# Kernel tuning notes

Hardware: AMD Instinct MI355X
Metric: run time of the kernel (lower is better)

The kernel has to match this reference:

```python
import jax, jax.numpy as jnp
import numpy as np

HOP = 768
NCB = 14
DIM = 512
VOCAB = 1024
W_SCALE = 0.02  # keep conv stacks numerically tame


def conv1d(x, w, b, stride=1, padding=0):
    # x: [B,C,L], w: [O,I,K] (torch layout), b: [O]
    y = jax.lax.conv_general_dilated(
        x, w, window_strides=(stride,), padding=[(padding, padding)],
        dimension_numbers=('NCH', 'OIH', 'NCH'))
    return y + b[None, :, None]


def conv_transpose1d(x, w, b, stride, padding):
    # torch ConvTranspose1d weight layout: (in, out, k)
    k = w.shape[2]
    w2 = jnp.flip(jnp.transpose(w, (1, 0, 2)), axis=2)  # -> OIH
    y = jax.lax.conv_general_dilated(
        x, w2, window_strides=(1,),
        padding=[(k - 1 - padding, k - 1 - padding)],
        lhs_dilation=(stride,),
        dimension_numbers=('NCH', 'OIH', 'NCH'))
    return y + b[None, :, None]


def setup_inputs() -> dict:
    key = jax.random.key(0)
    ks = jax.random.split(key, 16)
    f = lambda k, shp, s=W_SCALE: jax.random.normal(k, shp, dtype=jnp.float32) * s
    B, T = 2, 98304  # T = 768 * 128
    return {
        'audio': jax.random.normal(ks[0], (B, 1, T), dtype=jnp.float32),
        'codebooks': jax.random.normal(ks[1], (NCB, VOCAB, DIM), dtype=jnp.float32),
        'ew1': f(ks[2], (256, 1, 7)), 'eb1': f(ks[3], (256,)),
        'ew2': f(ks[4], (512, 256, 5)), 'eb2': f(ks[5], (512,)),
        'ew3': f(ks[6], (NCB * DIM, 512, 3)), 'eb3': f(ks[7], (NCB * DIM,)),
        'dw1': f(ks[8], (NCB * DIM, 512, 5)), 'db1': f(ks[9], (512,)),
        'dw2': f(ks[10], (256, 512, 5)), 'db2': f(ks[11], (256,)),
        'dw3': f(ks[12], (1, 256, 7)), 'db3': f(ks[13], (1,)),
    }


def reference(audio, codebooks, ew1, eb1, ew2, eb2, ew3, eb3,
              dw1, db1, dw2, db2, dw3, db3):
    B = audio.shape[0]
    # ---- encoder ----
    h = jax.nn.relu(conv1d(audio, ew1, eb1, stride=1, padding=3))
    h = jax.nn.relu(conv1d(h, ew2, eb2, stride=HOP, padding=2))
    h = conv1d(h, ew3, eb3, stride=1, padding=1)          # [B, NCB*DIM, S]
    S = h.shape[-1]
    emb = h.reshape(B, NCB, DIM, S).transpose(0, 1, 3, 2)  # [B, NCB, S, DIM]
    # ---- VQ: per-codebook squared L2 distance + argmin (same argmin as cdist) ----
    d2 = (jnp.sum(emb * emb, axis=-1, keepdims=True)            # [B,NCB,S,1]
          - 2.0 * jnp.einsum('bksd,kvd->bksv', emb, codebooks)  # [B,NCB,S,V]
          + jnp.sum(codebooks * codebooks, axis=-1)[None, :, None, :])
    codes = jnp.argmin(d2, axis=-1)                        # [B, NCB, S] int
    # ---- decode: embedding lookup + transposed conv decoder ----
    q = codebooks[jnp.arange(NCB)[None, :, None], codes]   # [B, NCB, S, DIM]
    q = q.transpose(0, 1, 3, 2).reshape(B, NCB * DIM, S)   # [B, NCB*DIM, S]
    a = jax.nn.relu(conv_transpose1d(q, dw1, db1, stride=HOP, padding=2))
    a = jax.nn.relu(conv1d(a, dw2, db2, stride=1, padding=2))
    a = jnp.tanh(conv1d(a, dw3, db3, stride=1, padding=3))
    return a  # [B, 1, (S-1)*HOP + 1]
```

## Files before the change

kernel.cpp:

```cpp
#include <hip/hip_runtime.h>
#include <hip/hip_bf16.h>
#include <math.h>

#define T_IN 98304
#define SS 128
#define NBATCH 2
#define NN 256
#define C1 256
#define C2 512
#define C3 7168
#define NCBK 14
#define DIMV 512
#define VOC 1024
#define TOUT 97537
#define HOP 768

#define OFF_CBN    0L
#define OFF_AB1    14336L
#define OFF_AB2    14848L
#define OFF_CCONST 15104L
#define OFF_H2C    15120L
#define OFF_H2XH   146192L
#define OFF_H2XL   342800L
#define OFF_H3H    539408L
#define OFF_H3L    1456912L
#define OFF_X1H    2374416L
#define OFF_X1L    2538256L
#define OFF_DW1T   539408L
#define OFF_XH     539408L
#define OFF_XL     3488528L
#define OFF_CODES  9714448L
#define OFF_QBF    9718032L
#define OFF_A1RAW  10635536L
#define OFF_DW2PH  10635536L
#define OFF_DW2PL  10963216L
#define OFF_A2ACT  11290896L
#define OFF_CBPH   11880720L
#define OFF_CBPL   15550736L
#define OFF_EW3PH  19220752L
#define OFF_EW3PL  24725776L
#define OFF_EW2PH  30230800L
#define OFF_EW2PL  30558480L
#define OFF_PVAL   30886160L
#define OFF_PIDX   30943504L

typedef __attribute__((ext_vector_type(8))) short short8;
typedef __attribute__((ext_vector_type(4))) float f32x4;

static __device__ inline ushort f2bf(float x) {
  __hip_bfloat16 h = __float2bfloat16(x);
  return *reinterpret_cast<ushort*>(&h);
}

static __device__ inline void split8(const float4 x0, const float4 x1,
                                     short8& h, short8& l) {
  float xs[8] = {x0.x, x0.y, x0.z, x0.w, x1.x, x1.y, x1.z, x1.w};
  #pragma unroll
  for (int e = 0; e < 8; ++e) {
    uint b = __float_as_uint(xs[e]);
    h[e] = (short)(b >> 16);
    float r = xs[e] - __uint_as_float(b & 0xffff0000u);
    l[e] = (short)(__float_as_uint(r) >> 16);
  }
}

__global__ __launch_bounds__(256) void k_cbp(const float* __restrict__ cb,
    ushort* __restrict__ ph, ushort* __restrict__ pl, float* __restrict__ cbn) {
  __shared__ float red[256];
  int zmt = blockIdx.x;
  int t = threadIdx.x;
  int lane = t & 63, fg = t >> 6;
  int quad = lane >> 4, l15 = lane & 15;
  int row = zmt * 16 + l15;
  float ss = 0.f;
  #pragma unroll
  for (int h = 0; h < 4; ++h) {
    int kt = fg * 4 + h;
    int k = kt * 32 + quad * 8;
    const float* s = cb + (long)row * DIMV + k;
    float4 x0 = *(const float4*)s;
    float4 x1 = *(const float4*)(s + 4);
    short8 hh, ll;
    split8(x0, x1, hh, ll);
    long off = ((long)zmt * 16 + kt) * 512 + lane * 8;
    *(short8*)(ph + off) = hh;
    *(short8*)(pl + off) = ll;
    ss += x0.x*x0.x + x0.y*x0.y + x0.z*x0.z + x0.w*x0.w
        + x1.x*x1.x + x1.y*x1.y + x1.z*x1.z + x1.w*x1.w;
  }
  red[t] = ss;
  __syncthreads();
  if (t < 16) {
    float s = 0.f;
    #pragma unroll
    for (int g = 0; g < 16; ++g) s += red[t + g * 16];
    cbn[zmt * 16 + t] = s;
  }
}

__global__ __launch_bounds__(256) void k_prep_ab2(const float* __restrict__ db1,
    const float* __restrict__ dw2, const float* __restrict__ db2,
    float* __restrict__ ab1, float* __restrict__ ab2) {
  __shared__ float red[256];
  int o = blockIdx.x, t = threadIdx.x;
  if (o == 0) { ab1[t] = fmaxf(db1[t], 0.f); ab1[t + 256] = fmaxf(db1[t + 256], 0.f); }
  const float* wp = dw2 + (long)o * C2 * 5;
  float acc = 0.f;
  #pragma unroll
  for (int h = 0; h < 2; ++h) {
    int c = t + h * 256;
    const float* p = wp + c * 5;
    float wsum = p[0] + p[1] + p[2] + p[3] + p[4];
    acc = fmaf(wsum, fmaxf(db1[c], 0.f), acc);
  }
  red[t] = acc;
  __syncthreads();
  for (int off = 128; off; off >>= 1) {
    if (t < off) red[t] += red[t + off];
    __syncthreads();
  }
  if (t == 0) ab2[o] = fmaxf(red[0] + db2[o], 0.f);
}

__global__ __launch_bounds__(256) void k_prep_c(const float* __restrict__ dw3,
    const float* __restrict__ db3, const float* __restrict__ ab2,
    float* __restrict__ cconst) {
  __shared__ float red[256];
  int t = threadIdx.x;
  float wsum3 = 0.f;
  #pragma unroll
  for (int j = 0; j < 7; ++j) wsum3 += dw3[t*7+j];
  red[t] = wsum3 * ab2[t];
  __syncthreads();
  for (int off = 128; off; off >>= 1) {
    if (t < off) red[t] += red[t + off];
    __syncthreads();
  }
  if (t == 0) cconst[0] = tanhf(red[0] + db3[0]);
}

__global__ __launch_bounds__(256) void k_enc1(const float* __restrict__ audio,
    const float* __restrict__ ew1, const float* __restrict__ eb1,
    ushort* __restrict__ X1h, ushort* __restrict__ X1l) {
  int n = blockIdx.x, ic = threadIdx.x;
  int b = n >> 7, s = n & 127;
  const float* ap = audio + (long)b * T_IN;
  int base = HOP * s - 5;
  float a[11];
  #pragma unroll
  for (int w = 0; w < 11; ++w) {
    int ai = base + w;
    a[w] = (ai >= 0 && ai < T_IN) ? ap[ai] : 0.f;
  }
  float w1[7];
  #pragma unroll
  for (int j = 0; j < 7; ++j) w1[j] = ew1[ic*7+j];
  float b1 = eb1[ic];
  #pragma unroll
  for (int jj = 0; jj < 5; ++jj) {
    int tcol = HOP * s + jj - 2;
    float v = 0.f;
    if (tcol >= 0) {
      float acc = b1;
      #pragma unroll
      for (int j = 0; j < 7; ++j) acc = fmaf(w1[j], a[jj + j], acc);
      v = fmaxf(acc, 0.f);
    }
    int k = ic * 5 + jj;
    int kt = k >> 5;
    int lane2 = ((k >> 3) & 3) * 16 + (n & 15);
    long idx = ((long)((n >> 4) * 40 + kt)) * 512 + lane2 * 8 + (k & 7);
    uint bi = __float_as_uint(v);
    X1h[idx] = (ushort)(bi >> 16);
    float r = v - __uint_as_float(bi & 0xffff0000u);
    X1l[idx] = (ushort)(__float_as_uint(r) >> 16);
  }
}

__global__ __launch_bounds__(256) void k_ew2p(const float* __restrict__ ew2,
    ushort* __restrict__ ph, ushort* __restrict__ pl) {
  int o8 = blockIdx.x * 256 + threadIdx.x;
  const int total = 512 * 1280 / 8;
  if (o8 >= total) return;
  int frag = o8 >> 6, lane = o8 & 63;
  int quad = lane >> 4, l15 = lane & 15;
  int mt = frag / 40, kt = frag - mt * 40;
  int m = mt * 16 + l15;
  int k = kt * 32 + quad * 8;
  const float* s = ew2 + (long)m * 1280 + k;
  float4 x0 = *(const float4*)s;
  float4 x1 = *(const float4*)(s + 4);
  short8 h, l;
  split8(x0, x1, h, l);
  long off = (long)o8 * 8;
  *(short8*)(ph + off) = h;
  *(short8*)(pl + off) = l;
}

__global__ __launch_bounds__(256) void gemm_enc2(const ushort* __restrict__ aH,
    const ushort* __restrict__ aL, const ushort* __restrict__ bH,
    const ushort* __restrict__ bL, const float* __restrict__ eb2,
    float* __restrict__ h2c) {
  __shared__ __align__(16) float red[4 * 2048];
  const int tid = threadIdx.x;
  const int w = tid >> 6, lane = tid & 63;
  const int l15 = lane & 15, quad = lane >> 4;
  const int m0 = blockIdx.x * 32, n0 = blockIdx.y * 64;
  const int mt0 = blockIdx.x * 2, nt0 = blockIdx.y * 4;
  const int kt0 = w * 10;
  f32x4 acc[2][4] = {};
  const ushort* aHB = aH + ((long)(mt0 * 40 + kt0)) * 512 + lane * 8;
  const ushort* aLB = aL + ((long)(mt0 * 40 + kt0)) * 512 + lane * 8;
  const ushort* bHB = bH + ((long)(nt0 * 40 + kt0)) * 512 + lane * 8;
  const ushort* bLB = bL + ((long)(nt0 * 40 + kt0)) * 512 + lane * 8;
  for (int kt = 0; kt < 10; ++kt) {
    short8 ah[2], al[2], bh[4], bl[4];
    #pragma unroll
    for (int i = 0; i < 2; ++i) {
      long o = ((long)(i * 40 + kt)) * 512;
      ah[i] = *(const short8*)(aHB + o);
      al[i] = *(const short8*)(aLB + o);
    }
    #pragma unroll
    for (int f = 0; f < 4; ++f) {
      long o = ((long)(f * 40 + kt)) * 512;
      bh[f] = *(const short8*)(bHB + o);
      bl[f] = *(const short8*)(bLB + o);
    }
    #pragma unroll
    for (int i = 0; i < 2; ++i)
      #pragma unroll
      for (int j = 0; j < 4; ++j) {
        acc[i][j] = __builtin_amdgcn_mfma_f32_16x16x32_bf16(ah[i], bh[j], acc[i][j], 0, 0, 0);
        acc[i][j] = __builtin_amdgcn_mfma_f32_16x16x32_bf16(ah[i], bl[j], acc[i][j], 0, 0, 0);
        acc[i][j] = __builtin_amdgcn_mfma_f32_16x16x32_bf16(al[i], bh[j], acc[i][j], 0, 0, 0);
      }
  }
  #pragma unroll
  for (int i = 0; i < 2; ++i)
    #pragma unroll
    for (int j = 0; j < 4; ++j)
      *(float4*)&red[w * 2048 + (i * 4 + j) * 256 + lane * 4] = *(float4*)&acc[i][j];
  __syncthreads();
  #pragma unroll
  for (int q = 0; q < 2; ++q) {
    const int c = 2 * w + q;
    const int i = c >> 2, j = c & 3;
    float4 s = make_float4(0.f, 0.f, 0.f, 0.f);
    #pragma unroll
    for (int g = 0; g < 4; ++g) {
      float4 t4 = *(const float4*)&red[g * 2048 + c * 256 + lane * 4];
      s.x += t4.x; s.y += t4.y; s.z += t4.z; s.w += t4.w;
    }
    const int obase = m0 + i * 16 + quad * 4;
    float4 bias = *(const float4*)(eb2 + obase);
    const int n = n0 + j * 16 + l15;
    float4 out;
    out.x = fmaxf(s.x + bias.x, 0.f);
    out.y = fmaxf(s.y + bias.y, 0.f);
    out.z = fmaxf(s.z + bias.z, 0.f);
    out.w = fmaxf(s.w + bias.w, 0.f);
    *(float4*)(h2c + (long)n * C2 + obase) = out;
  }
}

__global__ void k_h2x(const float* __restrict__ h2c, ushort* __restrict__ h2xph,
                      ushort* __restrict__ h2xpl) {
  int idx = blockIdx.x * 256 + threadIdx.x;
  const int total = NN * 1536;
  for (; idx < total; idx += gridDim.x * 256) {
    int grp = idx >> 9;
    int r = idx & 511;
    int e = r & 7, lane = r >> 3;
    int quad = lane >> 4, l15 = lane & 15;
    int nt = grp / 48, kt = grp - nt * 48;
    int n = nt * 16 + l15;
    int k = kt * 32 + quad * 8 + e;
    int ic = k / 3, j = k - ic * 3;
    int s2 = (n & 127) + j - 1;
    int b = n >> 7;
    float v = (s2 >= 0 && s2 < SS) ? h2c[(long)(b*SS + s2)*C2 + ic] : 0.f;
    uint bi = __float_as_uint(v);
    h2xph[idx] = (ushort)(bi >> 16);
    float rr = v - __uint_as_float(bi & 0xffff0000u);
    h2xpl[idx] = (ushort)(__float_as_uint(rr) >> 16);
  }
}

__global__ __launch_bounds__(256) void k_ew3p(const float* __restrict__ ew3,
    ushort* __restrict__ ph, ushort* __restrict__ pl) {
  int o8 = blockIdx.x * 256 + threadIdx.x;
  const int total = C3 * 1536 / 8;
  if (o8 >= total) return;
  int frag = o8 >> 6, lane = o8 & 63;
  int quad = lane >> 4, l15 = lane & 15;
  int mtL = frag / 48, kt = frag - mtL * 48;
  int m = mtL * 16 + l15;
  int k = kt * 32 + quad * 8;
  const float* s = ew3 + (long)m * 1536 + k;
  float4 x0 = *(const float4*)s;
  float4 x1 = *(const float4*)(s + 4);
  short8 h, l;
  split8(x0, x1, h, l);
  long off = (long)o8 * 8;
  *(short8*)(ph + off) = h;
  *(short8*)(pl + off) = l;
}

__global__ __launch_bounds__(256) void gemm_h3(const ushort* __restrict__ aH,
    const ushort* __restrict__ aL, const ushort* __restrict__ bH,
    const ushort* __restrict__ bL, const float* __restrict__ eb3,
    ushort* __restrict__ h3ph, ushort* __restrict__ h3pl) {
  __shared__ __align__(16) float red[4 * 4096];
  const int tid = threadIdx.x;
  const int w = tid >> 6, lane = tid & 63;
  const int l15 = lane & 15, quad = lane >> 4;
  const int bid = blockIdx.x;
  const int xcd = bid & 7, q = bid >> 3;
  const int mchunk = xcd * 14 + (q >> 2);
  const int nchunk = q & 3;
  const int mtL0 = mchunk * 4, nt0 = nchunk * 4, n0 = nchunk * 64;
  const int kt0 = w * 12;
  f32x4 acc[4][4] = {};
  const ushort* aHB = aH + ((long)(mtL0 * 48 + kt0)) * 512 + lane * 8;
  const ushort* aLB = aL + ((long)(mtL0 * 48 + kt0)) * 512 + lane * 8;
  const ushort* bHB = bH + ((long)(nt0 * 48 + kt0)) * 512 + lane * 8;
  const ushort* bLB = bL + ((long)(nt0 * 48 + kt0)) * 512 + lane * 8;
  for (int kt = 0; kt < 12; ++kt) {
    short8 ah[4], al[4], bh[4], bl[4];
    #pragma unroll
    for (int f = 0; f < 4; ++f) {
      long o = ((long)(f * 48 + kt)) * 512;
      ah[f] = *(const short8*)(aHB + o);
      al[f] = *(const short8*)(aLB + o);
      bh[f] = *(const short8*)(bHB + o);
      bl[f] = *(const short8*)(bLB + o);
    }
    #pragma unroll
    for (int i = 0; i < 4; ++i)
      #pragma unroll
      for (int j = 0; j < 4; ++j) {
        acc[i][j] = __builtin_amdgcn_mfma_f32_16x16x32_bf16(ah[i], bh[j], acc[i][j], 0, 0, 0);
        acc[i][j] = __builtin_amdgcn_mfma_f32_16x16x32_bf16(ah[i], bl[j], acc[i][j], 0, 0, 0);
        acc[i][j] = __builtin_amdgcn_mfma_f32_16x16x32_bf16(al[i], bh[j], acc[i][j], 0, 0, 0);
      }
  }
  #pragma unroll
  for (int i = 0; i < 4; ++i)
    #pragma unroll
    for (int j = 0; j < 4; ++j)
      *(float4*)&red[w * 4096 + (i * 4 + j) * 256 + lane * 4] = *(float4*)&acc[i][j];
  __syncthreads();
  const int mg0 = mchunk * 64 + w * 16 + quad * 4;
  float4 bias = *(const float4*)(eb3 + mg0);
  const int ktS = mg0 >> 5, quadk = (mg0 >> 3) & 3, es = mg0 & 7;
  #pragma unroll
  for (int j = 0; j < 4; ++j) {
    float4 s = *(const float4*)&red[(w * 4 + j) * 256 + lane * 4];
    #pragma unroll
    for (int r = 1; r < 4; ++r) {
      float4 tt = *(const float4*)&red[r * 4096 + (w * 4 + j) * 256 + lane * 4];
      s.x += tt.x; s.y += tt.y; s.z += tt.z; s.w += tt.w;
    }
    const int n = n0 + j * 16 + l15;
    float v0 = s.x + bias.x;
    float v1 = s.y + bias.y;
    float v2 = s.z + bias.z;
    float v3 = s.w + bias.w;
    uint b0 = __float_as_uint(v0), b1 = __float_as_uint(v1);
    uint b2 = __float_as_uint(v2), b3 = __float_as_uint(v3);
    uint2 hp;
    hp.x = (b0 >> 16) | (b1 & 0xffff0000u);
    hp.y = (b2 >> 16) | (b3 & 0xffff0000u);
    float r0 = v0 - __uint_as_float(b0 & 0xffff0000u);
    float r1 = v1 - __uint_as_float(b1 & 0xffff0000u);
    float r2 = v2 - __uint_as_float(b2 & 0xffff0000u);
    float r3 = v3 - __uint_as_float(b3 & 0xffff0000u);
    uint2 lp;
    lp.x = (__float_as_uint(r0) >> 16) | (__float_as_uint(r1) & 0xffff0000u);
    lp.y = (__float_as_uint(r2) >> 16) | (__float_as_uint(r3) & 0xffff0000u);
    long off = ((long)((n >> 4) * 224 + ktS)) * 512 + (quadk * 16 + (n & 15)) * 8 + es;
    *(uint2*)(h3ph + off) = hp;
    *(uint2*)(h3pl + off) = lp;
  }
}

__global__ __launch_bounds__(256) void gemm_scores(const ushort* __restrict__ aH,
    const ushort* __restrict__ aL, const ushort* __restrict__ bH,
    const ushort* __restrict__ bL, const float* __restrict__ cbn,
    float* __restrict__ pval, int* __restrict__ pidx) {
  __shared__ __align__(16) float red[4 * 4096];
  __shared__ float wv_[4 * 64];
  __shared__ int   wi_[4 * 64];
  const int tid = threadIdx.x;
  const int w = tid >> 6, lane = tid & 63;
  const int l15 = lane & 15, quad = lane >> 4;
  const int m0 = blockIdx.x * 64, n0 = blockIdx.y * 64, z = blockIdx.z;
  const int mt0 = blockIdx.x * 4;
  const int kt0 = w * 4;
  f32x4 acc[4][4] = {};
  const ushort* aHB = aH + ((long)((z * 64 + mt0) * 16 + kt0)) * 512 + lane * 8;
  const ushort* aLB = aL + ((long)((z * 64 + mt0) * 16 + kt0)) * 512 + lane * 8;
  const ushort* bHB = bH + ((long)((n0 >> 4) * 224 + z * 16 + kt0)) * 512 + lane * 8;
  const ushort* bLB = bL + ((long)((n0 >> 4) * 224 + z * 16 + kt0)) * 512 + lane * 8;
  for (int kt = 0; kt < 4; ++kt) {
    short8 ah[4], al[4], bh[4], bl[4];
    #pragma unroll
    for (int f = 0; f < 4; ++f) {
      long oa = ((long)(f * 16 + kt)) * 512;
      long ob = ((long)(f * 224 + kt)) * 512;
      ah[f] = *(const short8*)(aHB + oa);
      al[f] = *(const short8*)(aLB + oa);
      bh[f] = *(const short8*)(bHB + ob);
      bl[f] = *(const short8*)(bLB + ob);
    }
    #pragma unroll
    for (int i = 0; i < 4; ++i)
      #pragma unroll
      for (int j = 0; j < 4; ++j) {
        acc[i][j] = __builtin_amdgcn_mfma_f32_16x16x32_bf16(ah[i], bh[j], acc[i][j], 0, 0, 0);
        acc[i][j] = __builtin_amdgcn_mfma_f32_16x16x32_bf16(ah[i], bl[j], acc[i][j], 0, 0, 0);
        acc[i][j] = __builtin_amdgcn_mfma_f32_16x16x32_bf16(al[i], bh[j], acc[i][j], 0, 0, 0);
      }
  }
  #pragma unroll
  for (int i = 0; i < 4; ++i)
    #pragma unroll
    for (int j = 0; j < 4; ++j)
      *(float4*)&red[w * 4096 + (i * 4 + j) * 256 + lane * 4] = *(float4*)&acc[i][j];
  __syncthreads();
  const int vbase = m0 + w * 16 + quad * 4;
  float4 cn = *(const float4*)(cbn + z * VOC + vbase);
  #pragma unroll
  for (int j = 0; j < 4; ++j) {
    float4 s = *(const float4*)&red[(w * 4 + j) * 256 + lane * 4];
    #pragma unroll
    for (int r = 1; r < 4; ++r) {
      float4 tt = *(const float4*)&red[r * 4096 + (w * 4 + j) * 256 + lane * 4];
      s.x += tt.x; s.y += tt.y; s.z += tt.z; s.w += tt.w;
    }
    float o0 = cn.x - 2.f * s.x;
    float o1 = cn.y - 2.f * s.y;
    float o2 = cn.z - 2.f * s.z;
    float o3 = cn.w - 2.f * s.w;
    float bv = o0; int bm = vbase;
    if (o1 < bv) { bv = o1; bm = vbase + 1; }
    if (o2 < bv) { bv = o2; bm = vbase + 2; }
    if (o3 < bv) { bv = o3; bm = vbase + 3; }
    #pragma unroll
    for (int off = 16; off <= 32; off <<= 1) {
      float ov = __shfl_xor(bv, off);
      int om = __shfl_xor(bm, off);
      if (ov < bv || (ov == bv && om < bm)) { bv = ov; bm = om; }
    }
    if (quad == 0) { wv_[w * 64 + j * 16 + l15] = bv; wi_[w * 64 + j * 16 + l15] = bm; }
  }
  __syncthreads();
  if (tid < 64) {
    float bv = wv_[tid]; int bm = wi_[tid];
    #pragma unroll
    for (int g = 1; g < 4; ++g) {
      float ov = wv_[g * 64 + tid]; int om = wi_[g * 64 + tid];
      if (ov < bv || (ov == bv && om < bm)) { bv = ov; bm = om; }
    }
    long prow = (long)z * NN + n0 + tid;
    pval[prow * 16 + blockIdx.x] = bv;
    pidx[prow * 16 + blockIdx.x] = bm;
  }
}

__global__ void k_argmin2(const float* __restrict__ pval, const int* __restrict__ pidx,
                          int* __restrict__ codes) {
  int row = blockIdx.x * 256 + threadIdx.x;
  if (row >= NCBK * NN) return;
  const float* pv = pval + (long)row * 16;
  const int*   pi = pidx + (long)row * 16;
  float bv = pv[0]; int bm = pi[0];
  #pragma unroll
  for (int c = 1; c < 16; ++c) {
    float v = pv[c]; int m = pi[c];
    if (v < bv || (v == bv && m < bm)) { bv = v; bm = m; }
  }
  codes[row] = bm;
}

__global__ __launch_bounds__(256) void k_dw1t(const float* __restrict__ dw1,
                                              ushort* __restrict__ dw1p) {
  __shared__ __align__(16) ushort T[64 * 72];
  int t = threadIdx.x;
  int k0 = blockIdx.x * 64, m0 = blockIdx.y * 64;
  int kk = t >> 2, mj = (t & 3) * 16;
  const float* src = dw1 + (long)(k0 + kk) * 2560 + m0 + mj;
  float x[16];
  *(float4*)&x[0]  = *(const float4*)(src);
  *(float4*)&x[4]  = *(const float4*)(src + 4);
  *(float4*)&x[8]  = *(const float4*)(src + 8);
  *(float4*)&x[12] = *(const float4*)(src + 12);
  #pragma unroll
  for (int l = 0; l < 16; ++l)
    T[(mj + l) * 72 + kk] = f2bf(x[l]);
  __syncthreads();
  int mo = t >> 2, kc = (t & 3) * 16;
  const int m = m0 + mo;
  const int mt = m >> 4, l15 = m & 15;
  #pragma unroll
  for (int h = 0; h < 2; ++h) {
    const int kk0 = kc + h * 8;
    const int kglob = k0 + kk0;
    const int kt = kglob >> 5;
    const int quad = (kglob >> 3) & 3;
    uint4 u = *(const uint4*)&T[mo * 72 + kk0];
    *(uint4*)(dw1p + ((long)(mt * 224 + kt)) * 512 + (quad * 16 + l15) * 8) = u;
  }
}

__global__ void k_gather_qbf(const float* __restrict__ cb, const int* __restrict__ codes,
                             ushort* __restrict__ qp) {
  int o = blockIdx.x * 256 + threadIdx.x;
  const int total = NN * C3 / 8;
  if (o >= total) return;
  int frag = o >> 6, r = o & 63;
  int quad = r >> 4, l15 = r & 15;
  int nt = frag / 224, kt = frag - nt * 224;
  int n = nt * 16 + l15;
  int kglob = kt * 32 + quad * 8;
  int kcb = kglob >> 9, d0 = kglob & 511;
  int code = codes[kcb * NN + n];
  const float* s = cb + ((long)(kcb * VOC + code)) * DIMV + d0;
  float4 x0 = *(const float4*)s;
  float4 x1 = *(const float4*)(s + 4);
  uint4 u;
  u.x = (uint)f2bf(x0.x) | ((uint)f2bf(x0.y) << 16);
  u.y = (uint)f2bf(x0.z) | ((uint)f2bf(x0.w) << 16);
  u.z = (uint)f2bf(x1.x) | ((uint)f2bf(x1.y) << 16);
  u.w = (uint)f2bf(x1.z) | ((uint)f2bf(x1.w) << 16);
  ((uint4*)qp)[o] = u;
}

__global__ __launch_bounds__(1024) void gemm_a1_mfma(const ushort* __restrict__ dw1p,
    const ushort* __restrict__ qp, float* __restrict__ a1raw) {
  __shared__ __align__(16) float red[4 * 4096];
  const int tid = threadIdx.x;
  const int w = tid >> 6, lane = tid & 63;
  const int l15 = lane & 15, quad = lane >> 4;
  const int mt0 = blockIdx.x * 4, nt0 = blockIdx.y * 4;
  const int kt0 = w * 14;
  f32x4 acc[4][4] = {};
  const ushort* aB = dw1p + ((long)(mt0 * 224 + kt0)) * 512 + lane * 8;
  const ushort* bB = qp   + ((long)(nt0 * 224 + kt0)) * 512 + lane * 8;
  #pragma unroll 2
  for (int kt = 0; kt < 14; ++kt) {
    short8 ah[4], bh[4];
    #pragma unroll
    for (int f = 0; f < 4; ++f) {
      ah[f] = *(const short8*)(aB + ((long)(f * 224 + kt)) * 512);
      bh[f] = *(const short8*)(bB + ((long)(f * 224 + kt)) * 512);
    }
    #pragma unroll
    for (int i = 0; i < 4; ++i)
      #pragma unroll
      for (int j = 0; j < 4; ++j)
        acc[i][j] = __builtin_amdgcn_mfma_f32_16x16x32_bf16(ah[i], bh[j], acc[i][j], 0, 0, 0);
  }
  float4 rsum = make_float4(0.f, 0.f, 0.f, 0.f);
  #pragma unroll
  for (int r = 0; r < 4; ++r) {
    if ((w >> 2) == r) {
      #pragma unroll
      for (int i = 0; i < 4; ++i)
        #pragma unroll
        for (int j = 0; j < 4; ++j)
          *(float4*)&red[(w & 3) * 4096 + (i * 4 + j) * 256 + lane * 4] = *(float4*)&acc[i][j];
    }
    __syncthreads();
    #pragma unroll
    for (int g = 0; g < 4; ++g) {
      float4 t4 = *(const float4*)&red[g * 4096 + w * 256 + lane * 4];
      rsum.x += t4.x; rsum.y += t4.y; rsum.z += t4.z; rsum.w += t4.w;
    }
    __syncthreads();
  }
  const int ci = w >> 2, cj = w & 3;
  const int n = nt0 * 16 + cj * 16 + l15;
  const int mb = mt0 * 16 + ci * 16 + quad * 4;
  float v[4] = {rsum.x, rsum.y, rsum.z, rsum.w};
  #pragma unroll
  for (int reg = 0; reg < 4; ++reg) {
    int m = mb + reg;
    int c = m / 5, jj = m - c * 5;
    a1raw[((long)(n * 5 + jj)) * C2 + c] = v[reg];
  }
}

__global__ void k_x2(const float* __restrict__ a1raw, const float* __restrict__ ab1g,
                     const float* __restrict__ db1, ushort* __restrict__ Xh,
                     ushort* __restrict__ Xl) {
  int idx = blockIdx.x * 256 + threadIdx.x;
  const int total = 2304 * 2560;
  for (; idx < total; idx += gridDim.x * 256) {
    int grp = idx >> 9;
    int r = idx & 511;
    int e = r & 7, lane = r >> 3;
    int quad = lane >> 4, l15 = lane & 15;
    int nt = grp / 80, kt = grp - nt * 80;
    int nu = nt * 16 + l15;
    int ck = kt * 32 + quad * 8 + e;
    int n = nu / 9, u = nu - n * 9;
    int c = ck / 5, jj = ck - c * 5;
    int w = u + jj;
    int s = n & 127;
    int tc = HOP * s - 6 + w;
    float v;
    if (tc < 0 || tc > TOUT - 1) v = 0.f;
    else if (w >= 4 && w <= 8)
      v = fmaxf(db1[c] + a1raw[((long)(n * 5 + (w - 4))) * C2 + c], 0.f);
    else v = ab1g[c];
    uint bi = __float_as_uint(v);
    Xh[idx] = (ushort)(bi >> 16);
    float rr = v - __uint_as_float(bi & 0xffff0000u);
    Xl[idx] = (ushort)(__float_as_uint(rr) >> 16);
  }
}

__global__ __launch_bounds__(256) void k_dw2p(const float* __restrict__ dw2,
    ushort* __restrict__ ph, ushort* __restrict__ pl) {
  int o8 = blockIdx.x * 256 + threadIdx.x;
  const int total = 256 * 2560 / 8;
  if (o8 >= total) return;
  int frag = o8 >> 6, lane = o8 & 63;
  int quad = lane >> 4, l15 = lane & 15;
  int mt = frag / 80, kt = frag - mt * 80;
  int m = mt * 16 + l15;
  int k = kt * 32 + quad * 8;
  const float* s = dw2 + (long)m * 2560 + k;
  float4 x0 = *(const float4*)s;
  float4 x1 = *(const float4*)(s + 4);
  short8 h, l;
  split8(x0, x1, h, l);
  long off = (long)o8 * 8;
  *(short8*)(ph + off) = h;
  *(short8*)(pl + off) = l;
}

__global__ __launch_bounds__(256) void gemm_dec2(const ushort* __restrict__ aH,
    const ushort* __restrict__ aL, const ushort* __restrict__ bH,
    const ushort* __restrict__ bL, const float* __restrict__ db2,
    float* __restrict__ a2act) {
  __shared__ __align__(16) float red[4 * 4096];
  const int tid = threadIdx.x;
  const int w = tid >> 6, lane = tid & 63;
  const int l15 = lane & 15, quad = lane >> 4;
  const int mt0 = blockIdx.x * 4, nt0 = blockIdx.y * 4;
  const int m0 = mt0 * 16, n0 = nt0 * 16;
  const int kt0 = w * 20;
  f32x4 acc[4][4] = {};
  const ushort* aHB = aH + ((long)(mt0 * 80 + kt0)) * 512 + lane * 8;
  const ushort* aLB = aL + ((long)(mt0 * 80 + kt0)) * 512 + lane * 8;
  const ushort* bHB = bH + ((long)(nt0 * 80 + kt0)) * 512 + lane * 8;
  const ushort* bLB = bL + ((long)(nt0 * 80 + kt0)) * 512 + lane * 8;
  for (int kt = 0; kt < 20; ++kt) {
    short8 ah[4], al[4], bh[4], bl[4];
    #pragma unroll
    for (int f = 0; f < 4; ++f) {
      long o = ((long)(f * 80 + kt)) * 512;
      ah[f] = *(const short8*)(aHB + o);
      al[f] = *(const short8*)(aLB + o);
      bh[f] = *(const short8*)(bHB + o);
      bl[f] = *(const short8*)(bLB + o);
    }
    #pragma unroll
    for (int i = 0; i < 4; ++i)
      #pragma unroll
      for (int j = 0; j < 4; ++j) {
        acc[i][j] = __builtin_amdgcn_mfma_f32_16x16x32_bf16(ah[i], bh[j], acc[i][j], 0, 0, 0);
        acc[i][j] = __builtin_amdgcn_mfma_f32_16x16x32_bf16(ah[i], bl[j], acc[i][j], 0, 0, 0);
        acc[i][j] = __builtin_amdgcn_mfma_f32_16x16x32_bf16(al[i], bh[j], acc[i][j], 0, 0, 0);
      }
  }
  #pragma unroll
  for (int i = 0; i < 4; ++i)
    #pragma unroll
    for (int j = 0; j < 4; ++j)
      *(float4*)&red[w * 4096 + (i * 4 + j) * 256 + lane * 4] = *(float4*)&acc[i][j];
  __syncthreads();
  const int mb = m0 + w * 16 + quad * 4;
  float4 bias = *(const float4*)(db2 + mb);
  #pragma unroll
  for (int j = 0; j < 4; ++j) {
    float4 s = *(const float4*)&red[(w * 4 + j) * 256 + lane * 4];
    #pragma unroll
    for (int r = 1; r < 4; ++r) {
      float4 tt = *(const float4*)&red[r * 4096 + (w * 4 + j) * 256 + lane * 4];
      s.x += tt.x; s.y += tt.y; s.z += tt.z; s.w += tt.w;
    }
    const int nu = n0 + j * 16 + l15;
    float4 out;
    out.x = fmaxf(s.x + bias.x, 0.f);
    out.y = fmaxf(s.y + bias.y, 0.f);
    out.z = fmaxf(s.z + bias.z, 0.f);
    out.w = fmaxf(s.w + bias.w, 0.f);
    *(float4*)(a2act + (long)nu * C1 + mb) = out;
  }
}

__global__ void k_fill(float* __restrict__ outp, const float* __restrict__ cconst) {
  float v = cconst[0];
  int idx = blockIdx.x * 256 + threadIdx.x;
  const int total = NBATCH * TOUT;
  for (; idx < total; idx += gridDim.x * 256) outp[idx] = v;
}

__global__ __launch_bounds__(256) void k_dec3(const float* __restrict__ a2act,
    const float* __restrict__ ab2g, const float* __restrict__ dw3,
    const float* __restrict__ db3, float* __restrict__ outp) {
  __shared__ float sa2[9 * C1];
  __shared__ float sb[C1];
  int n = blockIdx.x;
  int s = n & 127, b = n >> 7;
  int t = threadIdx.x;
  for (int i = t; i < 9 * C1; i += 256) sa2[i] = a2act[(long)n * 9 * C1 + i];
  sb[t] = ab2g[t];
  __syncthreads();
  int wv = t >> 6, lane = t & 63;
  float b3 = db3[0];
  for (int w15 = wv; w15 < 15; w15 += 4) {
    int tc = HOP * s - 7 + w15;
    if (tc < 0 || tc > TOUT - 1) continue;
    float part = 0.f;
    for (int cc = lane; cc < C1; cc += 64) {
      #pragma unroll
      for (int j = 0; j < 7; ++j) {
        int wcol = tc + j - 3;
        float x;
        if (wcol < 0 || wcol > TOUT - 1) x = 0.f;
        else {
          int du = wcol - (HOP * s - 4);
          x = (du >= 0 && du <= 8) ? sa2[du * C1 + cc] : sb[cc];
        }
        part = fmaf(dw3[cc*7+j], x, part);
      }
    }
    for (int off = 32; off; off >>= 1) part += __shfl_down(part, off);
    if (lane == 0) outp[(long)b * TOUT + tc] = tanhf(part + b3);
  }
}

extern "C" void kernel_launch(void* const* d_in, const int* in_sizes, int n_in,
                              void* d_out, int out_size, void* d_ws, size_t ws_size,
                              hipStream_t stream) {
  const float* audio = (const float*)d_in[0];
  const float* cb    = (const float*)d_in[1];
  const float* ew1   = (const float*)d_in[2];
  const float* eb1   = (const float*)d_in[3];
  const float* ew2   = (const float*)d_in[4];
  const float* eb2   = (const float*)d_in[5];
  const float* ew3   = (const float*)d_in[6];
  const float* eb3   = (const float*)d_in[7];
  const float* dw1   = (const float*)d_in[8];
  const float* db1   = (const float*)d_in[9];
  const float* dw2   = (const float*)d_in[10];
  const float* db2   = (const float*)d_in[11];
  const float* dw3   = (const float*)d_in[12];
  const float* db3   = (const float*)d_in[13];
  float* outp = (float*)d_out;
  float* ws = (float*)d_ws;

  float*  cbn    = ws + OFF_CBN;
  float*  ab1    = ws + OFF_AB1;
  float*  ab2    = ws + OFF_AB2;
  float*  cconst = ws + OFF_CCONST;
  float*  h2c    = ws + OFF_H2C;
  ushort* h2xph  = (ushort*)(ws + OFF_H2XH);
  ushort* h2xpl  = (ushort*)(ws + OFF_H2XL);
  ushort* h3ph   = (ushort*)(ws + OFF_H3H);
  ushort* h3pl   = (ushort*)(ws + OFF_H3L);
  ushort* X1h    = (ushort*)(ws + OFF_X1H);
  ushort* X1l    = (ushort*)(ws + OFF_X1L);
  ushort* cbph   = (ushort*)(ws + OFF_CBPH);
  ushort* cbpl   = (ushort*)(ws + OFF_CBPL);
  ushort* ew3ph  = (ushort*)(ws + OFF_EW3PH);
  ushort* ew3pl  = (ushort*)(ws + OFF_EW3PL);
  ushort* ew2ph  = (ushort*)(ws + OFF_EW2PH);
  ushort* ew2pl  = (ushort*)(ws + OFF_EW2PL);
  float*  pval   = ws + OFF_PVAL;
  int*    pidx   = (int*)(ws + OFF_PIDX);
  ushort* dw1p   = (ushort*)(ws + OFF_DW1T);
  ushort* Xh     = (ushort*)(ws + OFF_XH);
  ushort* Xl     = (ushort*)(ws + OFF_XL);
  int*    codes  = (int*)(ws + OFF_CODES);
  ushort* qp     = (ushort*)(ws + OFF_QBF);
  float*  a1raw  = ws + OFF_A1RAW;
  ushort* dw2ph  = (ushort*)(ws + OFF_DW2PH);
  ushort* dw2pl  = (ushort*)(ws + OFF_DW2PL);
  float*  a2act  = ws + OFF_A2ACT;

  k_cbp<<<896, 256, 0, stream>>>(cb, cbph, cbpl, cbn);
  k_prep_ab2<<<C1, 256, 0, stream>>>(db1, dw2, db2, ab1, ab2);
  k_prep_c<<<1, 256, 0, stream>>>(dw3, db3, ab2, cconst);
  k_enc1<<<NN, 256, 0, stream>>>(audio, ew1, eb1, X1h, X1l);
  k_ew2p<<<320, 256, 0, stream>>>(ew2, ew2ph, ew2pl);
  gemm_enc2<<<dim3(16, 4), 256, 0, stream>>>(ew2ph, ew2pl, X1h, X1l, eb2, h2c);
  k_h2x<<<384, 256, 0, stream>>>(h2c, h2xph, h2xpl);
  k_ew3p<<<5376, 256, 0, stream>>>(ew3, ew3ph, ew3pl);
  gemm_h3<<<448, 256, 0, stream>>>(ew3ph, ew3pl, h2xph, h2xpl, eb3, h3ph, h3pl);
  gemm_scores<<<dim3(16, 4, 14), 256, 0, stream>>>(cbph, cbpl, h3ph, h3pl, cbn, pval, pidx);
  k_argmin2<<<14, 256, 0, stream>>>(pval, pidx, codes);
  k_dw1t<<<dim3(112, 40), 256, 0, stream>>>(dw1, dw1p);
  k_gather_qbf<<<896, 256, 0, stream>>>(cb, codes, qp);
  gemm_a1_mfma<<<dim3(40, 4), 1024, 0, stream>>>(dw1p, qp, a1raw);
  k_x2<<<4096, 256, 0, stream>>>(a1raw, ab1, db1, Xh, Xl);
  k_dw2p<<<320, 256, 0, stream>>>(dw2, dw2ph, dw2pl);
  gemm_dec2<<<dim3(4, 36), 256, 0, stream>>>(dw2ph, dw2pl, Xh, Xl, db2, a2act);
  k_fill<<<256, 256, 0, stream>>>(outp, cconst);
  k_dec3<<<NN, 256, 0, stream>>>(a2act, ab2, dw3, db3, outp);
}
```

Baseline: 389.3 us.

## Merge weight-packing kernels, fuse output fill into dec3, widen dec2 split-K

The five separate weight-packing kernels (codebook, ew2, ew3, dw2, dw1 transpose) are merged into one large launch that branches on block index, and their workspace regions are moved so they no longer alias. The standalone constant-fill kernel is folded into k_dec3, where each block writes the fill value over its own output span. gemm_dec2 now uses 1024 threads with a 16-way K split and a staged shared-memory reduction, adding wave parallelism per tile. Together these cut launch count and serial dependencies, at the cost of more barriers in the dec2 reduction and a larger workspace footprint.

```diff
diff --git a/kernel.cpp b/kernel.cpp
--- a/kernel.cpp
+++ b/kernel.cpp
@@ -26,14 +26,11 @@
 #define OFF_H3L    1456912L
 #define OFF_X1H    2374416L
 #define OFF_X1L    2538256L
-#define OFF_DW1T   539408L
 #define OFF_XH     539408L
 #define OFF_XL     3488528L
 #define OFF_CODES  9714448L
 #define OFF_QBF    9718032L
 #define OFF_A1RAW  10635536L
-#define OFF_DW2PH  10635536L
-#define OFF_DW2PL  10963216L
 #define OFF_A2ACT  11290896L
 #define OFF_CBPH   11880720L
 #define OFF_CBPL   15550736L
@@ -43,6 +40,9 @@
 #define OFF_EW2PL  30558480L
 #define OFF_PVAL   30886160L
 #define OFF_PIDX   30943504L
+#define OFF_DW1P   31000848L
+#define OFF_DW2PH  40175888L
+#define OFF_DW2PL  40503568L
 
 typedef __attribute__((ext_vector_type(8))) short short8;
 typedef __attribute__((ext_vector_type(4))) float f32x4;
@@ -64,37 +64,113 @@
   }
 }
 
-__global__ __launch_bounds__(256) void k_cbp(const float* __restrict__ cb,
-    ushort* __restrict__ ph, ushort* __restrict__ pl, float* __restrict__ cbn) {
+__global__ __launch_bounds__(256) void k_packw(const float* __restrict__ cb,
+    const float* __restrict__ ew2, const float* __restrict__ ew3,
+    const float* __restrict__ dw2, const float* __restrict__ dw1,
+    ushort* __restrict__ cbph, ushort* __restrict__ cbpl, float* __restrict__ cbn,
+    ushort* __restrict__ ew2ph, ushort* __restrict__ ew2pl,
+    ushort* __restrict__ ew3ph, ushort* __restrict__ ew3pl,
+    ushort* __restrict__ dw2ph, ushort* __restrict__ dw2pl,
+    ushort* __restrict__ dw1p) {
+  __shared__ __align__(16) ushort T[64 * 72];
   __shared__ float red[256];
-  int zmt = blockIdx.x;
-  int t = threadIdx.x;
-  int lane = t & 63, fg = t >> 6;
-  int quad = lane >> 4, l15 = lane & 15;
-  int row = zmt * 16 + l15;
-  float ss = 0.f;
-  #pragma unroll
-  for (int h = 0; h < 4; ++h) {
-    int kt = fg * 4 + h;
-    int k = kt * 32 + quad * 8;
-    const float* s = cb + (long)row * DIMV + k;
+  const int bid = blockIdx.x;
+  const int t = threadIdx.x;
+  if (bid < 896) {
+    int zmt = bid;
+    int lane = t & 63, fg = t >> 6;
+    int quad = lane >> 4, l15 = lane & 15;
+    int row = zmt * 16 + l15;
+    float ss = 0.f;
+    #pragma unroll
+    for (int h = 0; h < 4; ++h) {
+      int kt = fg * 4 + h;
+      int k = kt * 32 + quad * 8;
+      const float* s = cb + (long)row * DIMV + k;
+      float4 x0 = *(const float4*)s;
+      float4 x1 = *(const float4*)(s + 4);
+      short8 hh, ll;
+      split8(x0, x1, hh, ll);
+      long off = ((long)zmt * 16 + kt) * 512 + lane * 8;
+      *(short8*)(cbph + off) = hh;
+      *(short8*)(cbpl + off) = ll;
+      ss += x0.x*x0.x + x0.y*x0.y + x0.z*x0.z + x0.w*x0.w
+          + x1.x*x1.x + x1.y*x1.y + x1.z*x1.z + x1.w*x1.w;
+    }
+    red[t] = ss;
+    __syncthreads();
+    if (t < 16) {
+      float s = 0.f;
+      #pragma unroll
+      for (int g = 0; g < 16; ++g) s += red[t + g * 16];
+      cbn[zmt * 16 + t] = s;
+    }
+  } else if (bid < 1216) {
+    int o8 = (bid - 896) * 256 + t;
+    int frag = o8 >> 6, lane = o8 & 63;
+    int quad = lane >> 4, l15 = lane & 15;
+    int mt = frag / 40, kt = frag - mt * 40;
+    const float* s = ew2 + (long)(mt * 16 + l15) * 1280 + kt * 32 + quad * 8;
     float4 x0 = *(const float4*)s;
     float4 x1 = *(const float4*)(s + 4);
-    short8 hh, ll;
-    split8(x0, x1, hh, ll);
-    long off = ((long)zmt * 16 + kt) * 512 + lane * 8;
-    *(short8*)(ph + off) = hh;
-    *(short8*)(pl + off) = ll;
-    ss += x0.x*x0.x + x0.y*x0.y + x0.z*x0.z + x0.w*x0.w
-        + x1.x*x1.x + x1.y*x1.y + x1.z*x1.z + x1.w*x1.w;
-  }
-  red[t] = ss;
-  __syncthreads();
-  if (t < 16) {
-    float s = 0.f;
-    #pragma unroll
-    for (int g = 0; g < 16; ++g) s += red[t + g * 16];
-    cbn[zmt * 16 + t] = s;
+    short8 h, l;
+    split8(x0, x1, h, l);
+    long off = (long)o8 * 8;
+    *(short8*)(ew2ph + off) = h;
+    *(short8*)(ew2pl + off) = l;
+  } else if (bid < 6592) {
+    int o8 = (bid - 1216) * 256 + t;
+    int frag = o8 >> 6, lane = o8 & 63;
+    int quad = lane >> 4, l15 = lane & 15;
+    int mtL = frag / 48, kt = frag - mtL * 48;
+    const float* s = ew3 + (long)(mtL * 16 + l15) * 1536 + kt * 32 + quad * 8;
+    float4 x0 = *(const float4*)s;
+    float4 x1 = *(const float4*)(s + 4);
+    short8 h, l;
+    split8(x0, x1, h, l);
+    long off = (long)o8 * 8;
+    *(short8*)(ew3ph + off) = h;
+    *(short8*)(ew3pl + off) = l;
+  } else if (bid < 6912) {
+    int o8 = (bid - 6592) * 256 + t;
+    int frag = o8 >> 6, lane = o8 & 63;
+    int quad = lane >> 4, l15 = lane & 15;
+    int mt = frag / 80, kt = frag - mt * 80;
+    const float* s = dw2 + (long)(mt * 16 + l15) * 2560 + kt * 32 + quad * 8;
+    float4 x0 = *(const float4*)s;
+    float4 x1 = *(const float4*)(s + 4);
+    short8 h, l;
+    split8(x0, x1, h, l);
+    long off = (long)o8 * 8;
+    *(short8*)(dw2ph + off) = h;
+    *(short8*)(dw2pl + off) = l;
+  } else {
+    int idx = bid - 6912;
+    int kb = idx / 40, mb = idx - kb * 40;
+    int k0 = kb * 64, m0 = mb * 64;
+    int kk = t >> 2, mj = (t & 3) * 16;
+    const float* src = dw1 + (long)(k0 + kk) * 2560 + m0 + mj;
+    float x[16];
+    *(float4*)&x[0]  = *(const float4*)(src);
+    *(float4*)&x[4]  = *(const float4*)(src + 4);
+    *(float4*)&x[8]  = *(const float4*)(src + 8);
+    *(float4*)&x[12] = *(const float4*)(src + 12);
+    #pragma unroll
+    for (int l = 0; l < 16; ++l)
+      T[(mj + l) * 72 + kk] = f2bf(x[l]);
+    __syncthreads();
+    int mo = t >> 2, kc = (t & 3) * 16;
+    const int m = m0 + mo;
+    const int mt = m >> 4, l15 = m & 15;
+    #pragma unroll
+    for (int h = 0; h < 2; ++h) {
+      const int kk0 = kc + h * 8;
+      const int kglob = k0 + kk0;
+      const int kt = kglob >> 5;
+      const int quad = (kglob >> 3) & 3;
+      uint4 u = *(const uint4*)&T[mo * 72 + kk0];
+      *(uint4*)(dw1p + ((long)(mt * 224 + kt)) * 512 + (quad * 16 + l15) * 8) = u;
+    }
   }
 }
 
@@ -175,26 +251,6 @@
     float r = v - __uint_as_float(bi & 0xffff0000u);
     X1l[idx] = (ushort)(__float_as_uint(r) >> 16);
   }
-}
-
-__global__ __launch_bounds__(256) void k_ew2p(const float* __restrict__ ew2,
-    ushort* __restrict__ ph, ushort* __restrict__ pl) {
-  int o8 = blockIdx.x * 256 + threadIdx.x;
-  const int total = 512 * 1280 / 8;
-  if (o8 >= total) return;
-  int frag = o8 >> 6, lane = o8 & 63;
-  int quad = lane >> 4, l15 = lane & 15;
-  int mt = frag / 40, kt = frag - mt * 40;
-  int m = mt * 16 + l15;
-  int k = kt * 32 + quad * 8;
-  const float* s = ew2 + (long)m * 1280 + k;
-  float4 x0 = *(const float4*)s;
-  float4 x1 = *(const float4*)(s + 4);
-  short8 h, l;
-  split8(x0, x1, h, l);
-  long off = (long)o8 * 8;
-  *(short8*)(ph + off) = h;
-  *(short8*)(pl + off) = l;
 }
 
 __global__ __launch_bounds__(256) void gemm_enc2(const ushort* __restrict__ aH,
@@ -285,26 +341,6 @@
     float rr = v - __uint_as_float(bi & 0xffff0000u);
     h2xpl[idx] = (ushort)(__float_as_uint(rr) >> 16);
   }
-}
-
-__global__ __launch_bounds__(256) void k_ew3p(const float* __restrict__ ew3,
-    ushort* __restrict__ ph, ushort* __restrict__ pl) {
-  int o8 = blockIdx.x * 256 + threadIdx.x;
-  const int total = C3 * 1536 / 8;
-  if (o8 >= total) return;
-  int frag = o8 >> 6, lane = o8 & 63;
-  int quad = lane >> 4, l15 = lane & 15;
-  int mtL = frag / 48, kt = frag - mtL * 48;
-  int m = mtL * 16 + l15;
-  int k = kt * 32 + quad * 8;
-  const float* s = ew3 + (long)m * 1536 + k;
-  float4 x0 = *(const float4*)s;
-  float4 x1 = *(const float4*)(s + 4);
-  short8 h, l;
-  split8(x0, x1, h, l);
-  long off = (long)o8 * 8;
-  *(short8*)(ph + off) = h;
-  *(short8*)(pl + off) = l;
 }
 
 __global__ __launch_bounds__(256) void gemm_h3(const ushort* __restrict__ aH,
@@ -482,36 +518,6 @@
     if (v < bv || (v == bv && m < bm)) { bv = v; bm = m; }
   }
   codes[row] = bm;
-}
-
-__global__ __launch_bounds__(256) void k_dw1t(const float* __restrict__ dw1,
-                                              ushort* __restrict__ dw1p) {
-  __shared__ __align__(16) ushort T[64 * 72];
-  int t = threadIdx.x;
-  int k0 = blockIdx.x * 64, m0 = blockIdx.y * 64;
-  int kk = t >> 2, mj = (t & 3) * 16;
-  const float* src = dw1 + (long)(k0 + kk) * 2560 + m0 + mj;
-  float x[16];
-  *(float4*)&x[0]  = *(const float4*)(src);
-  *(float4*)&x[4]  = *(const float4*)(src + 4);
-  *(float4*)&x[8]  = *(const float4*)(src + 8);
-  *(float4*)&x[12] = *(const float4*)(src + 12);
-  #pragma unroll
-  for (int l = 0; l < 16; ++l)
-    T[(mj + l) * 72 + kk] = f2bf(x[l]);
-  __syncthreads();
-  int mo = t >> 2, kc = (t & 3) * 16;
-  const int m = m0 + mo;
-  const int mt = m >> 4, l15 = m & 15;
-  #pragma unroll
-  for (int h = 0; h < 2; ++h) {
-    const int kk0 = kc + h * 8;
-    const int kglob = k0 + kk0;
-    const int kt = kglob >> 5;
-    const int quad = (kglob >> 3) & 3;
-    uint4 u = *(const uint4*)&T[mo * 72 + kk0];
-    *(uint4*)(dw1p + ((long)(mt * 224 + kt)) * 512 + (quad * 16 + l15) * 8) = u;
-  }
 }
 
 __global__ void k_gather_qbf(const float* __restrict__ cb, const int* __restrict__ codes,
@@ -622,27 +628,7 @@
   }
 }
 
-__global__ __launch_bounds__(256) void k_dw2p(const float* __restrict__ dw2,
-    ushort* __restrict__ ph, ushort* __restrict__ pl) {
-  int o8 = blockIdx.x * 256 + threadIdx.x;
-  const int total = 256 * 2560 / 8;
-  if (o8 >= total) return;
-  int frag = o8 >> 6, lane = o8 & 63;
-  int quad = lane >> 4, l15 = lane & 15;
-  int mt = frag / 80, kt = frag - mt * 80;
-  int m = mt * 16 + l15;
-  int k = kt * 32 + quad * 8;
-  const float* s = dw2 + (long)m * 2560 + k;
-  float4 x0 = *(const float4*)s;
-  float4 x1 = *(const float4*)(s + 4);
-  short8 h, l;
-  split8(x0, x1, h, l);
-  long off = (long)o8 * 8;
-  *(short8*)(ph + off) = h;
-  *(short8*)(pl + off) = l;
-}
-
-__global__ __launch_bounds__(256) void gemm_dec2(const ushort* __restrict__ aH,
+__global__ __launch_bounds__(1024) void gemm_dec2(const ushort* __restrict__ aH,
     const ushort* __restrict__ aL, const ushort* __restrict__ bH,
     const ushort* __restrict__ bL, const float* __restrict__ db2,
     float* __restrict__ a2act) {
@@ -651,14 +637,13 @@
   const int w = tid >> 6, lane = tid & 63;
   const int l15 = lane & 15, quad = lane >> 4;
   const int mt0 = blockIdx.x * 4, nt0 = blockIdx.y * 4;
-  const int m0 = mt0 * 16, n0 = nt0 * 16;
-  const int kt0 = w * 20;
+  const int kt0 = w * 5;
   f32x4 acc[4][4] = {};
   const ushort* aHB = aH + ((long)(mt0 * 80 + kt0)) * 512 + lane * 8;
   const ushort* aLB = aL + ((long)(mt0 * 80 + kt0)) * 512 + lane * 8;
   const ushort* bHB = bH + ((long)(nt0 * 80 + kt0)) * 512 + lane * 8;
   const ushort* bLB = bL + ((long)(nt0 * 80 + kt0)) * 512 + lane * 8;
-  for (int kt = 0; kt < 20; ++kt) {
+  for (int kt = 0; kt < 5; ++kt) {
     short8 ah[4], al[4], bh[4], bl[4];
     #pragma unroll
     for (int f = 0; f < 4; ++f) {
@@ -677,42 +662,40 @@
         acc[i][j] = __builtin_amdgcn_mfma_f32_16x16x32_bf16(al[i], bh[j], acc[i][j], 0, 0, 0);
       }
   }
-  #pragma unroll
-  for (int i = 0; i < 4; ++i)
-    #pragma unroll
-    for (int j = 0; j < 4; ++j)
-      *(float4*)&red[w * 4096 + (i * 4 + j) * 256 + lane * 4] = *(float4*)&acc[i][j];
-  __syncthreads();
-  const int mb = m0 + w * 16 + quad * 4;
+  float4 rsum = make_float4(0.f, 0.f, 0.f, 0.f);
+  #pragma unroll
+  for (int r = 0; r < 4; ++r) {
+    if ((w >> 2) == r) {
+      #pragma unroll
+      for (int i = 0; i < 4; ++i)
+        #pragma unroll
+        for (int j = 0; j < 4; ++j)
+          *(float4*)&red[(w & 3) * 4096 + (i * 4 + j) * 256 + lane * 4] = *(float4*)&acc[i][j];
+    }
+    __syncthreads();
+    #pragma unroll
+    for (int g = 0; g < 4; ++g) {
+      float4 t4 = *(const float4*)&red[g * 4096 + w * 256 + lane * 4];
+      rsum.x += t4.x; rsum.y += t4.y; rsum.z += t4.z; rsum.w += t4.w;
+    }
+    __syncthreads();
+  }
+  const int ci = w >> 2, cj = w & 3;
+  const int n = nt0 * 16 + cj * 16 + l15;
+  const int mb = mt0 * 16 + ci * 16 + quad * 4;
   float4 bias = *(const float4*)(db2 + mb);
-  #pragma unroll
-  for (int j = 0; j < 4; ++j) {
-    float4 s = *(const float4*)&red[(w * 4 + j) * 256 + lane * 4];
-    #pragma unroll
-    for (int r = 1; r < 4; ++r) {
-      float4 tt = *(const float4*)&red[r * 4096 + (w * 4 + j) * 256 + lane * 4];
-      s.x += tt.x; s.y += tt.y; s.z += tt.z; s.w += tt.w;
-    }
-    const int nu = n0 + j * 16 + l15;
-    float4 out;
-    out.x = fmaxf(s.x + bias.x, 0.f);
-    out.y = fmaxf(s.y + bias.y, 0.f);
-    out.z = fmaxf(s.z + bias.z, 0.f);
-    out.w = fmaxf(s.w + bias.w, 0.f);
-    *(float4*)(a2act + (long)nu * C1 + mb) = out;
-  }
-}
-
-__global__ void k_fill(float* __restrict__ outp, const float* __restrict__ cconst) {
-  float v = cconst[0];
-  int idx = blockIdx.x * 256 + threadIdx.x;
-  const int total = NBATCH * TOUT;
-  for (; idx < total; idx += gridDim.x * 256) outp[idx] = v;
+  float4 out;
+  out.x = fmaxf(rsum.x + bias.x, 0.f);
+  out.y = fmaxf(rsum.y + bias.y, 0.f);
+  out.z = fmaxf(rsum.z + bias.z, 0.f);
+  out.w = fmaxf(rsum.w + bias.w, 0.f);
+  *(float4*)(a2act + (long)n * C1 + mb) = out;
 }
 
 __global__ __launch_bounds__(256) void k_dec3(const float* __restrict__ a2act,
     const float* __restrict__ ab2g, const float* __restrict__ dw3,
-    const float* __restrict__ db3, float* __restrict__ outp) {
+    const float* __restrict__ db3, const float* __restrict__ cconst,
+    float* __restrict__ outp) {
   __shared__ float sa2[9 * C1];
   __shared__ float sb[C1];
   int n = blockIdx.x;
@@ -721,6 +704,13 @@
   for (int i = t; i < 9 * C1; i += 256) sa2[i] = a2act[(long)n * 9 * C1 + i];
   sb[t] = ab2g[t];
   __syncthreads();
+  float vfill = cconst[0];
+  int lo = (s == 0) ? 0 : HOP * s - 384;
+  int hi = (s == SS - 1) ? TOUT : HOP * s + 384;
+  for (int tc = lo + t; tc < hi; tc += 256) {
+    int d = tc - HOP * s;
+    if (d < -7 || d > 7) outp[(long)b * TOUT + tc] = vfill;
+  }
   int wv = t >> 6, lane = t & 63;
   float b3 = db3[0];
   for (int w15 = wv; w15 < 15; w15 += 4) {
@@ -784,33 +774,29 @@
   ushort* ew2pl  = (ushort*)(ws + OFF_EW2PL);
   float*  pval   = ws + OFF_PVAL;
   int*    pidx   = (int*)(ws + OFF_PIDX);
-  ushort* dw1p   = (ushort*)(ws + OFF_DW1T);
+  ushort* dw1p   = (ushort*)(ws + OFF_DW1P);
+  ushort* dw2ph  = (ushort*)(ws + OFF_DW2PH);
+  ushort* dw2pl  = (ushort*)(ws + OFF_DW2PL);
   ushort* Xh     = (ushort*)(ws + OFF_XH);
   ushort* Xl     = (ushort*)(ws + OFF_XL);
   int*    codes  = (int*)(ws + OFF_CODES);
   ushort* qp     = (ushort*)(ws + OFF_QBF);
   float*  a1raw  = ws + OFF_A1RAW;
-  ushort* dw2ph  = (ushort*)(ws + OFF_DW2PH);
-  ushort* dw2pl  = (ushort*)(ws + OFF_DW2PL);
   float*  a2act  = ws + OFF_A2ACT;
 
-  k_cbp<<<896, 256, 0, stream>>>(cb, cbph, cbpl, cbn);
+  k_packw<<<11392, 256, 0, stream>>>(cb, ew2, ew3, dw2, dw1,
+      cbph, cbpl, cbn, ew2ph, ew2pl, ew3ph, ew3pl, dw2ph, dw2pl, dw1p);
   k_prep_ab2<<<C1, 256, 0, stream>>>(db1, dw2, db2, ab1, ab2);
   k_prep_c<<<1, 256, 0, stream>>>(dw3, db3, ab2, cconst);
   k_enc1<<<NN, 256, 0, stream>>>(audio, ew1, eb1, X1h, X1l);
-  k_ew2p<<<320, 256, 0, stream>>>(ew2, ew2ph, ew2pl);
   gemm_enc2<<<dim3(16, 4), 256, 0, stream>>>(ew2ph, ew2pl, X1h, X1l, eb2, h2c);
   k_h2x<<<384, 256, 0, stream>>>(h2c, h2xph, h2xpl);
-  k_ew3p<<<5376, 256, 0, stream>>>(ew3, ew3ph, ew3pl);
   gemm_h3<<<448, 256, 0, stream>>>(ew3ph, ew3pl, h2xph, h2xpl, eb3, h3ph, h3pl);
   gemm_scores<<<dim3(16, 4, 14), 256, 0, stream>>>(cbph, cbpl, h3ph, h3pl, cbn, pval, pidx);
   k_argmin2<<<14, 256, 0, stream>>>(pval, pidx, codes);
-  k_dw1t<<<dim3(112, 40), 256, 0, stream>>>(dw1, dw1p);
   k_gather_qbf<<<896, 256, 0, stream>>>(cb, codes, qp);
   gemm_a1_mfma<<<dim3(40, 4), 1024, 0, stream>>>(dw1p, qp, a1raw);
   k_x2<<<4096, 256, 0, stream>>>(a1raw, ab1, db1, Xh, Xl);
-  k_dw2p<<<320, 256, 0, stream>>>(dw2, dw2ph, dw2pl);
-  gemm_dec2<<<dim3(4, 36), 256, 0, stream>>>(dw2ph, dw2pl, Xh, Xl, db2, a2act);
-  k_fill<<<256, 256, 0, stream>>>(outp, cconst);
-  k_dec3<<<NN, 256, 0, stream>>>(a2act, ab2, dw3, db3, outp);
-}
+  gemm_dec2<<<dim3(4, 36), 1024, 0, stream>>>(dw2ph, dw2pl, Xh, Xl, db2, a2act);
+  k_dec3<<<NN, 256, 0, stream>>>(a2act, ab2, dw3, db3, cconst, outp);
+}
```

Result: no change. 391.0 us (+0.4%).
